# Kernel tuning notes

Measured on AMD Instinct MI355X. Metric: run time of the kernel, lower is better.

Reference implementation:

```python
import jax, jax.numpy as jnp
import numpy as np

SR = 16000
N_TAPS = 10
MIN_F = 50.0
MAX_F = 2000.0


def setup_inputs() -> dict:
    key = jax.random.key(0)
    k1, k2 = jax.random.split(key)
    x = jax.random.normal(k1, (8, 1, 32000), dtype=jnp.float32)
    # raw f params as in the module: 3*(rand*2-1) in [-3, 3]
    f = 3.0 * (jax.random.uniform(k2, (128, 1), dtype=jnp.float32) * 2.0 - 1.0)
    a = jnp.full((128, 1), 0.9, dtype=jnp.float32)
    return {"x": x, "f": f, "a": a}


def _comb(x, f_raw, a):
    # scaling_function (min_freq/max_freq branch, no bins):
    # f = min_freq * (max_freq/min_freq) ** sigmoid(f_raw)
    fratio = MAX_F / MIN_F
    f = MIN_F * fratio ** jax.nn.sigmoid(f_raw)  # [O, I] fundamental freq in Hz

    B, I, T = x.shape
    O = f.shape[0]
    D = SR / f  # [O, I] fractional delay in samples (one period)
    n = jnp.arange(T, dtype=x.dtype)
    ci = jnp.arange(I)[None, :, None]  # channel index for gather, [1, I, 1]

    acc = jnp.zeros((B, O, T), dtype=x.dtype)
    # y[b,o,t] = sum_i sum_{k=0}^{n_taps-1} a[o,i]^k * lerp(x[b,i, t - k*D[o,i]])
    for k in range(N_TAPS):
        pos = n[None, None, :] - k * D[:, :, None]  # [O, I, T] fractional read positions
        i0 = jnp.floor(pos)
        frac = (pos - i0).astype(x.dtype)
        valid = (i0 >= 0).astype(x.dtype)  # causal: zero before signal start
        i0i = jnp.clip(i0.astype(jnp.int32), 0, T - 1)
        i1i = jnp.clip(i0i + 1, 0, T - 1)
        x0 = x[:, ci, i0i]  # [B, O, I, T]
        x1 = x[:, ci, i1i]  # [B, O, I, T]
        tap = (x0 * (1.0 - frac) + x1 * frac) * valid
        acc = acc + jnp.sum((a ** k)[None, :, :, None] * tap, axis=2)
    return acc


def reference(x, f, a):
    # use_bias=False -> b = 0, gain g unused in forward
    return _comb(x, f, a)
```

## Files before the change

### kernel.cpp

```cpp
#include <hip/hip_runtime.h>
#include <math.h>

#define T_LEN 32000
#define B_N 8
#define O_N 128
#define NTAPS 10
#define TILE_T 1280
#define PAD 2944
#define NSTAGE (TILE_T + PAD + 1)
#define NSTAGE_AL ((NSTAGE + 3) & ~3)
#define OCHUNK 8
#define TC 640

__global__ __launch_bounds__(128) void comb_params_kernel(
    const float* __restrict__ f, const float* __restrict__ a,
    float* __restrict__ tp) {
  int o = threadIdx.x;
  double fr = (double)f[o];
  double sig = 1.0 / (1.0 + exp(-fr));
  float ff = (float)(50.0 * pow(40.0, sig));
  float D = 16000.0f / ff;
  float av = a[o];
  for (int k = 0; k < NTAPS; ++k) {
    tp[o * 20 + k] = (float)k * D;
    tp[o * 20 + 10 + k] = (float)pow((double)av, (double)k);
  }
}

#define LOAD_PARAMS                                                        \
  const float4* p4 = (const float4*)(tp + (oc + oi) * 20);                 \
  float4 q0 = p4[0], q1 = p4[1], q2 = p4[2], q3 = p4[3], q4 = p4[4];       \
  float kD[NTAPS] = {q0.x, q0.y, q0.z, q0.w, q1.x,                         \
                     q1.y, q1.z, q1.w, q2.x, q2.y};                        \
  float ak[NTAPS] = {q2.z, q2.w, q3.x, q3.y, q3.z,                         \
                     q3.w, q4.x, q4.y, q4.z, q4.w};

__device__ __forceinline__ void comb_body_fast(const float* __restrict__ tp,
                                               float* __restrict__ outp,
                                               const float2* sx2, int oc,
                                               int t0, int tid) {
  float tcf = (float)(t0 + TC);
  int cbase = PAD - t0 - TC + 5 * tid;
  int b0 = PAD + 5 * tid;
  float2 A0 = sx2[b0], B0 = sx2[b0 + 2], C0 = sx2[b0 + 4];
#pragma unroll 1
  for (int oi = 0; oi < OCHUNK; ++oi) {
    LOAD_PARAMS
    float acc[5] = {A0.x, A0.y, B0.x, B0.y, C0.x};
#pragma unroll
    for (int k = 1; k < NTAPS; ++k) {
      float pc = tcf - kD[k];
      float fc = __builtin_amdgcn_fractf(pc);
      int sb = (int)(pc - fc) + cbase;
      float w1 = ak[k] * fc;
      float w0 = ak[k] - w1;
      float2 A = sx2[sb];
      float2 B = sx2[sb + 2];
      float2 C = sx2[sb + 4];
      acc[0] = fmaf(w0, A.x, fmaf(w1, A.y, acc[0]));
      acc[1] = fmaf(w0, A.y, fmaf(w1, B.x, acc[1]));
      acc[2] = fmaf(w0, B.x, fmaf(w1, B.y, acc[2]));
      acc[3] = fmaf(w0, B.y, fmaf(w1, C.x, acc[3]));
      acc[4] = fmaf(w0, C.x, fmaf(w1, C.y, acc[4]));
    }
#pragma unroll
    for (int u = 0; u < 5; ++u) outp[(size_t)oi * T_LEN + u] = acc[u];
  }
}

__device__ __forceinline__ void comb_body_edge(const float* __restrict__ tp,
                                               float* __restrict__ outp,
                                               const float2* sx2, int oc,
                                               int t0, int tid, int base_g) {
  float tf[5];
#pragma unroll
  for (int u = 0; u < 5; ++u) tf[u] = (float)(t0 + 5 * tid + u);
#pragma unroll 1
  for (int oi = 0; oi < OCHUNK; ++oi) {
    LOAD_PARAMS
    float acc[5];
#pragma unroll
    for (int u = 0; u < 5; ++u) acc[u] = 0.0f;
#pragma unroll
    for (int k = 0; k < NTAPS; ++k) {
#pragma unroll
      for (int u = 0; u < 5; ++u) {
        float pos = tf[u] - kD[k];
        float frac = __builtin_amdgcn_fractf(pos);
        int idx = (int)pos - base_g;
        float2 xv = sx2[idx];
        float tap = fmaf(frac, xv.y - xv.x, xv.x);
        tap = (pos >= 0.0f) ? tap : 0.0f;
        acc[u] = fmaf(ak[k], tap, acc[u]);
      }
    }
#pragma unroll
    for (int u = 0; u < 5; ++u) outp[(size_t)oi * T_LEN + u] = acc[u];
  }
}

__global__ __launch_bounds__(256) void comb_main_kernel(
    const float* __restrict__ x, const float* __restrict__ tp,
    float* __restrict__ out) {
  __shared__ float2 sx2[NSTAGE_AL];
  int bx = blockIdx.x;
  int t0 = bx * TILE_T;
  int b = blockIdx.y;
  int oc = blockIdx.z * OCHUNK;
  const float* __restrict__ xrow = x + b * T_LEN;
  int base_g = t0 - PAD;
  int tid = threadIdx.x;

  if (bx >= 3 && bx <= 23) {
    const float4* g4 = (const float4*)(xrow + base_g);
#pragma unroll 1
    for (int j = tid; j < NSTAGE_AL / 4; j += 256) {
      float4 v = g4[j];
      float nx = xrow[base_g + 4 * j + 4];
      sx2[4 * j + 0] = make_float2(v.x, v.y);
      sx2[4 * j + 1] = make_float2(v.y, v.z);
      sx2[4 * j + 2] = make_float2(v.z, v.w);
      sx2[4 * j + 3] = make_float2(v.w, nx);
    }
  } else {
#pragma unroll 1
    for (int j = tid; j < NSTAGE_AL; j += 256) {
      int g = base_g + j;
      float v0 = 0.0f, v1 = 0.0f;
      if (g >= 0) v0 = xrow[g < T_LEN - 1 ? g : T_LEN - 1];
      if (g + 1 >= 0) v1 = xrow[g + 1 < T_LEN - 1 ? g + 1 : T_LEN - 1];
      sx2[j] = make_float2(v0, v1);
    }
  }
  __syncthreads();

  float* outp = out + ((size_t)b * O_N + oc) * T_LEN + t0 + 5 * tid;

  if (bx >= 3) {
    comb_body_fast(tp, outp, sx2, oc, t0, tid);
  } else {
    comb_body_edge(tp, outp, sx2, oc, t0, tid, base_g);
  }
}

extern "C" void kernel_launch(void* const* d_in, const int* in_sizes, int n_in,
                              void* d_out, int out_size, void* d_ws,
                              size_t ws_size, hipStream_t stream) {
  const float* x = (const float*)d_in[0];
  const float* f = (const float*)d_in[1];
  const float* a = (const float*)d_in[2];
  float* out = (float*)d_out;
  float* tp = (float*)d_ws;

  comb_params_kernel<<<1, 128, 0, stream>>>(f, a, tp);

  dim3 grid(T_LEN / TILE_T, B_N, O_N / OCHUNK);
  comb_main_kernel<<<grid, 256, 0, stream>>>(x, tp, out);
}
```

Measured before the change: 169.5 us.

## Raise outputs per thread to eight with float4 stores and skewed LDS layout

Each thread now computes eight consecutive outputs instead of five, so TILE_T grows to 2048 and the grid shrinks to 16 time tiles, with a partial last tile whose excess threads skip their stores. Shared-memory indexing gains a skew (one pad slot per 16) to spread bank accesses, and outputs are written as two float4 stores. Staging handles the new boundary tile with a mixed vectorized and clamped path. The aim is to amortize the per-tap weight math over more outputs and cut global store instructions, at the cost of more registers, idle lanes in the last tile, and fewer blocks overall.

```diff
diff --git a/kernel.cpp b/kernel.cpp
--- a/kernel.cpp
+++ b/kernel.cpp
@@ -5,12 +5,16 @@
 #define B_N 8
 #define O_N 128
 #define NTAPS 10
-#define TILE_T 1280
+#define NTHREADS 256
+#define UT 8
+#define TILE_T (NTHREADS * UT)
 #define PAD 2944
 #define NSTAGE (TILE_T + PAD + 1)
 #define NSTAGE_AL ((NSTAGE + 3) & ~3)
+#define SK(p) ((p) + ((p) >> 4))
+#define NSLOTS (NSTAGE_AL + (NSTAGE_AL >> 4))
 #define OCHUNK 8
-#define TC 640
+#define TC 1024
 
 __global__ __launch_bounds__(128) void comb_params_kernel(
     const float* __restrict__ f, const float* __restrict__ a,
@@ -38,15 +42,16 @@
 __device__ __forceinline__ void comb_body_fast(const float* __restrict__ tp,
                                                float* __restrict__ outp,
                                                const float2* sx2, int oc,
-                                               int t0, int tid) {
+                                               int t0, int tid, bool do_store) {
   float tcf = (float)(t0 + TC);
-  int cbase = PAD - t0 - TC + 5 * tid;
-  int b0 = PAD + 5 * tid;
-  float2 A0 = sx2[b0], B0 = sx2[b0 + 2], C0 = sx2[b0 + 4];
+  int cbase = PAD - t0 - TC + UT * tid;
+  int b0 = PAD + UT * tid;
+  float2 A0 = sx2[SK(b0)], B0 = sx2[SK(b0 + 2)];
+  float2 C0 = sx2[SK(b0 + 4)], D0 = sx2[SK(b0 + 6)];
 #pragma unroll 1
   for (int oi = 0; oi < OCHUNK; ++oi) {
     LOAD_PARAMS
-    float acc[5] = {A0.x, A0.y, B0.x, B0.y, C0.x};
+    float acc[UT] = {A0.x, A0.y, B0.x, B0.y, C0.x, C0.y, D0.x, D0.y};
 #pragma unroll
     for (int k = 1; k < NTAPS; ++k) {
       float pc = tcf - kD[k];
@@ -54,17 +59,25 @@
       int sb = (int)(pc - fc) + cbase;
       float w1 = ak[k] * fc;
       float w0 = ak[k] - w1;
-      float2 A = sx2[sb];
-      float2 B = sx2[sb + 2];
-      float2 C = sx2[sb + 4];
+      float2 A = sx2[SK(sb)];
+      float2 B = sx2[SK(sb + 2)];
+      float2 C = sx2[SK(sb + 4)];
+      float2 D = sx2[SK(sb + 6)];
+      float2 E = sx2[SK(sb + 8)];
       acc[0] = fmaf(w0, A.x, fmaf(w1, A.y, acc[0]));
       acc[1] = fmaf(w0, A.y, fmaf(w1, B.x, acc[1]));
       acc[2] = fmaf(w0, B.x, fmaf(w1, B.y, acc[2]));
       acc[3] = fmaf(w0, B.y, fmaf(w1, C.x, acc[3]));
       acc[4] = fmaf(w0, C.x, fmaf(w1, C.y, acc[4]));
+      acc[5] = fmaf(w0, C.y, fmaf(w1, D.x, acc[5]));
+      acc[6] = fmaf(w0, D.x, fmaf(w1, D.y, acc[6]));
+      acc[7] = fmaf(w0, D.y, fmaf(w1, E.x, acc[7]));
     }
-#pragma unroll
-    for (int u = 0; u < 5; ++u) outp[(size_t)oi * T_LEN + u] = acc[u];
+    if (do_store) {
+      float4* o4 = (float4*)(outp + (size_t)oi * T_LEN);
+      o4[0] = make_float4(acc[0], acc[1], acc[2], acc[3]);
+      o4[1] = make_float4(acc[4], acc[5], acc[6], acc[7]);
+    }
   }
 }
 
@@ -72,37 +85,38 @@
                                                float* __restrict__ outp,
                                                const float2* sx2, int oc,
                                                int t0, int tid, int base_g) {
-  float tf[5];
+  float tf[UT];
 #pragma unroll
-  for (int u = 0; u < 5; ++u) tf[u] = (float)(t0 + 5 * tid + u);
+  for (int u = 0; u < UT; ++u) tf[u] = (float)(t0 + UT * tid + u);
 #pragma unroll 1
   for (int oi = 0; oi < OCHUNK; ++oi) {
     LOAD_PARAMS
-    float acc[5];
+    float acc[UT];
 #pragma unroll
-    for (int u = 0; u < 5; ++u) acc[u] = 0.0f;
+    for (int u = 0; u < UT; ++u) acc[u] = 0.0f;
 #pragma unroll
     for (int k = 0; k < NTAPS; ++k) {
 #pragma unroll
-      for (int u = 0; u < 5; ++u) {
+      for (int u = 0; u < UT; ++u) {
         float pos = tf[u] - kD[k];
         float frac = __builtin_amdgcn_fractf(pos);
         int idx = (int)pos - base_g;
-        float2 xv = sx2[idx];
+        float2 xv = sx2[SK(idx)];
         float tap = fmaf(frac, xv.y - xv.x, xv.x);
         tap = (pos >= 0.0f) ? tap : 0.0f;
         acc[u] = fmaf(ak[k], tap, acc[u]);
       }
     }
-#pragma unroll
-    for (int u = 0; u < 5; ++u) outp[(size_t)oi * T_LEN + u] = acc[u];
+    float4* o4 = (float4*)(outp + (size_t)oi * T_LEN);
+    o4[0] = make_float4(acc[0], acc[1], acc[2], acc[3]);
+    o4[1] = make_float4(acc[4], acc[5], acc[6], acc[7]);
   }
 }
 
 __global__ __launch_bounds__(256) void comb_main_kernel(
     const float* __restrict__ x, const float* __restrict__ tp,
     float* __restrict__ out) {
-  __shared__ float2 sx2[NSTAGE_AL];
+  __shared__ float2 sx2[NSLOTS];
   int bx = blockIdx.x;
   int t0 = bx * TILE_T;
   int b = blockIdx.y;
@@ -111,33 +125,53 @@
   int base_g = t0 - PAD;
   int tid = threadIdx.x;
 
-  if (bx >= 3 && bx <= 23) {
+  if (bx >= 2 && bx <= 14) {
     const float4* g4 = (const float4*)(xrow + base_g);
 #pragma unroll 1
-    for (int j = tid; j < NSTAGE_AL / 4; j += 256) {
-      float4 v = g4[j];
-      float nx = xrow[base_g + 4 * j + 4];
-      sx2[4 * j + 0] = make_float2(v.x, v.y);
-      sx2[4 * j + 1] = make_float2(v.y, v.z);
-      sx2[4 * j + 2] = make_float2(v.z, v.w);
-      sx2[4 * j + 3] = make_float2(v.w, nx);
+    for (int jq = tid; jq < NSTAGE_AL / 4; jq += 256) {
+      float4 v = g4[jq];
+      float nx = xrow[base_g + 4 * jq + 4];
+      int p = 4 * jq;
+      sx2[SK(p)]     = make_float2(v.x, v.y);
+      sx2[SK(p + 1)] = make_float2(v.y, v.z);
+      sx2[SK(p + 2)] = make_float2(v.z, v.w);
+      sx2[SK(p + 3)] = make_float2(v.w, nx);
+    }
+  } else if (bx == 15) {
+    const float4* g4 = (const float4*)(xrow + base_g);
+#pragma unroll 1
+    for (int jq = tid; jq < 1055; jq += 256) {
+      float4 v = g4[jq];
+      float nx = xrow[base_g + 4 * jq + 4];
+      int p = 4 * jq;
+      sx2[SK(p)]     = make_float2(v.x, v.y);
+      sx2[SK(p + 1)] = make_float2(v.y, v.z);
+      sx2[SK(p + 2)] = make_float2(v.z, v.w);
+      sx2[SK(p + 3)] = make_float2(v.w, nx);
+    }
+#pragma unroll 1
+    for (int p = 4220 + tid; p < NSTAGE_AL; p += 256) {
+      int g = base_g + p;
+      float v0 = xrow[g < T_LEN - 1 ? g : T_LEN - 1];
+      float v1 = xrow[g + 1 < T_LEN - 1 ? g + 1 : T_LEN - 1];
+      sx2[SK(p)] = make_float2(v0, v1);
     }
   } else {
 #pragma unroll 1
-    for (int j = tid; j < NSTAGE_AL; j += 256) {
-      int g = base_g + j;
+    for (int p = tid; p < NSTAGE_AL; p += 256) {
+      int g = base_g + p;
       float v0 = 0.0f, v1 = 0.0f;
       if (g >= 0) v0 = xrow[g < T_LEN - 1 ? g : T_LEN - 1];
       if (g + 1 >= 0) v1 = xrow[g + 1 < T_LEN - 1 ? g + 1 : T_LEN - 1];
-      sx2[j] = make_float2(v0, v1);
+      sx2[SK(p)] = make_float2(v0, v1);
     }
   }
   __syncthreads();
 
-  float* outp = out + ((size_t)b * O_N + oc) * T_LEN + t0 + 5 * tid;
+  float* outp = out + ((size_t)b * O_N + oc) * T_LEN + t0 + UT * tid;
 
-  if (bx >= 3) {
-    comb_body_fast(tp, outp, sx2, oc, t0, tid);
+  if (bx >= 2) {
+    comb_body_fast(tp, outp, sx2, oc, t0, tid, bx < 15 || tid < 160);
   } else {
     comb_body_edge(tp, outp, sx2, oc, t0, tid, base_g);
   }
@@ -154,6 +188,6 @@
 
   comb_params_kernel<<<1, 128, 0, stream>>>(f, a, tp);
 
-  dim3 grid(T_LEN / TILE_T, B_N, O_N / OCHUNK);
+  dim3 grid(16, B_N, O_N / OCHUNK);
   comb_main_kernel<<<grid, 256, 0, stream>>>(x, tp, out);
 }
```

New measurement: 237.1 us. 1.4x slower.
